# Performance work log

Hardware: AMD Instinct MI355X
Metric: run time of the kernel (lower is better)

The kernel has to match this reference:

```python
import jax, jax.numpy as jnp
import numpy as np

B, N, C = 2, 65536, 256
H, D, S = 8, 64, 64  # heads, dim_head, slice_num
INNER = H * D


def setup_inputs() -> dict:
    key = jax.random.key(0)
    ks = jax.random.split(key, 8)
    scale_in = 1.0 / np.sqrt(C)
    scale_d = 1.0 / np.sqrt(D)
    return {
        "x": jax.random.normal(ks[0], (B, N, C), dtype=jnp.float32),
        "W_x": jax.random.uniform(ks[1], (C, INNER), jnp.float32, -scale_in, scale_in),
        "b_x": jax.random.uniform(ks[2], (INNER,), jnp.float32, -scale_in, scale_in),
        "W_fx": jax.random.uniform(ks[3], (C, INNER), jnp.float32, -scale_in, scale_in),
        "b_fx": jax.random.uniform(ks[4], (INNER,), jnp.float32, -scale_in, scale_in),
        "W_slice": jax.random.uniform(ks[5], (D, S), jnp.float32, -scale_d, scale_d),
        "b_slice": jax.random.uniform(ks[6], (S,), jnp.float32, -scale_d, scale_d),
        "temperature": jnp.full((1, H, 1, 1), 0.5, dtype=jnp.float32),
    }


def _split_heads(t):
    # (B, N, H*D) -> (B, H, N, D)
    return t.reshape(B, N, H, D).transpose(0, 2, 1, 3)


def reference(x, W_x, b_x, W_fx, b_fx, W_slice, b_slice, temperature):
    projected_x = _split_heads(x @ W_x + b_x)          # (B,H,N,D)
    fx = _split_heads(x @ W_fx + b_fx)                 # (B,H,N,D)
    slice_proj = projected_x @ W_slice + b_slice       # (B,H,N,S)
    temp = jnp.clip(temperature, 0.5, 5.0)
    slice_weights = jax.nn.softmax(slice_proj / temp, axis=-1)  # (B,H,N,S)
    slice_norm = slice_weights.sum(axis=2)             # (B,H,S)
    normed = slice_weights / (slice_norm[:, :, None, :] + 0.01)
    # weighted token aggregation: (B,H,S,D)
    slice_tokens = jnp.einsum("bhns,bhnd->bhsd", normed, fx)
    return slice_tokens
```

## Files before the change

### kernel.cpp

```cpp
#include <hip/hip_runtime.h>

typedef _Float16 f16;
typedef __attribute__((ext_vector_type(8))) _Float16 f16x8;
typedef __attribute__((ext_vector_type(4))) _Float16 f16x4;
typedef __attribute__((ext_vector_type(4))) float    f32x4;

#define MFMA(a,b,c) __builtin_amdgcn_mfma_f32_16x16x32_f16(a,b,c,0,0,0)

constexpr int Bc = 2, Nc = 65536, Cc = 256, Hc = 8;
constexpr int CHUNK = 512;
constexpr int LDX = 72;
constexpr int LDT = 136;

constexpr size_t X16_OFF = 1048576;
constexpr size_t WS_BIG  = X16_OFF + (size_t)131072 * 256 * 2;

__device__ __forceinline__ f32x4 splat4(float v) { f32x4 r; r.x=v; r.y=v; r.z=v; r.w=v; return r; }
__device__ __forceinline__ f16x8 pack8(float4 a, float4 b) {
  f16x8 r = { (f16)a.x,(f16)a.y,(f16)a.z,(f16)a.w,(f16)b.x,(f16)b.y,(f16)b.z,(f16)b.w };
  return r;
}

__device__ __forceinline__ void gl_lds16(const f16* g, f16* l) {
  __builtin_amdgcn_global_load_lds((const __attribute__((address_space(1))) void*)g,
                                   (__attribute__((address_space(3))) void*)l, 16, 0, 0);
}
__device__ __forceinline__ void bar_lgkm() {
  asm volatile("s_waitcnt lgkmcnt(0)" ::: "memory");
  __builtin_amdgcn_s_barrier();
  __builtin_amdgcn_sched_barrier(0);
}
template<int N> __device__ __forceinline__ void bar_vm() {
  __builtin_amdgcn_sched_barrier(0);
  asm volatile("s_waitcnt vmcnt(%0)" :: "i"(N) : "memory");
  __builtin_amdgcn_s_barrier();
  __builtin_amdgcn_sched_barrier(0);
}

__global__ void prep_b(const float* __restrict__ x, const float* __restrict__ Wx,
                       const float* __restrict__ Wfx, const float* __restrict__ Wsl,
                       const float* __restrict__ bx, const float* __restrict__ bsl,
                       f16* __restrict__ WC, float* __restrict__ bsp,
                       float* __restrict__ Tz, f16* __restrict__ x16, int cvt_blocks) {
  __shared__ float tile[64][72];
  int b = blockIdx.x;
  const int t = threadIdx.x;
  if (b < cvt_blocks) {
    const long i = ((long)b * 256 + t) * 8;
    float4 a = *(const float4*)&x[i];
    float4 c = *(const float4*)&x[i + 4];
    *(f16x8*)&x16[i] = pack8(a, c);
    return;
  }
  b -= cvt_blocks;
  if (b < 32) {
    const int k0 = (b & 3) * 64, c0 = (b >> 2) * 64;
    const int r = t >> 4, c4 = (t & 15) * 4;
    #pragma unroll
    for (int i = 0; i < 4; ++i) {
      float4 v = *(const float4*)&Wfx[(size_t)(k0 + r + i*16)*512 + c0 + c4];
      tile[r + i*16][c4] = v.x; tile[r + i*16][c4+1] = v.y;
      tile[r + i*16][c4+2] = v.z; tile[r + i*16][c4+3] = v.w;
    }
    __syncthreads();
    const int cl = t >> 2, kq = t & 3;
    const int col = c0 + cl, h = col >> 6, n = col & 63;
    f16 tmp[16];
    #pragma unroll
    for (int jj = 0; jj < 16; ++jj) tmp[jj] = (f16)tile[kq*16 + jj][cl];
    f16* dst = WC + (size_t)(h*128 + n)*256 + k0 + kq*16;
    *(f16x8*)dst       = *(f16x8*)&tmp[0];
    *(f16x8*)(dst + 8) = *(f16x8*)&tmp[8];
  } else if (b < 96) {
    const int bb = b - 32;
    const int h = bb >> 3, k0 = (bb & 7) * 32;
    const int k = t & 31, sq = t >> 5;
    float accs[8];
    #pragma unroll
    for (int jj = 0; jj < 8; ++jj) accs[jj] = 0.f;
    for (int d = 0; d < 64; ++d) {
      float a = Wx[(size_t)(k0 + k)*512 + h*64 + d];
      #pragma unroll
      for (int jj = 0; jj < 8; ++jj) accs[jj] += a * Wsl[d*64 + sq*8 + jj];
    }
    #pragma unroll
    for (int jj = 0; jj < 8; ++jj)
      WC[(size_t)(h*128 + 64 + sq*8 + jj)*256 + k0 + k] = (f16)accs[jj];
  } else if (b == 96) {
    for (int u = t; u < 512; u += 256) {
      int h = u >> 6, s = u & 63;
      float a = bsl[s];
      for (int d = 0; d < 64; ++d) a += bx[h*64 + d] * Wsl[d*64 + s];
      bsp[h*64 + s] = a;
    }
  } else {
    float4 z; z.x = z.y = z.z = z.w = 0.f;
    ((float4*)Tz)[(b - 97) * 256 + t] = z;
  }
}

__global__ __launch_bounds__(256, 1)
void fused_dma(const f16* __restrict__ x16, const float* __restrict__ bfx,
               const float* __restrict__ bsp, const float* __restrict__ temp,
               const f16* __restrict__ WC,   float* __restrict__ Tg,
               float* __restrict__ normg) {
  __shared__ alignas(1024) f16 smem[32768];
  f16* X0 = smem;          f16* W0 = smem +  8192;
  f16* X1 = smem + 16384;  f16* W1 = smem + 24576;
  f16* sm_fxT = X1;
  f16* sm_wT  = W1;

  const int j    = blockIdx.x;
  const int xcd  = j & 7, slot = j >> 3;
  const int chunk = xcd * 32 + (slot >> 3);
  const int h     = slot & 7;

  const int tid = threadIdx.x;
  const int wv = tid >> 6, lane = tid & 63, quad = lane >> 4, ln = lane & 15;
  const int wm = wv >> 1, wn = wv & 1;
  const long tokBase = (long)chunk * CHUNK;
  const int b  = (int)(tokBase >> 16);
  const int bh = b * Hc + h;

  const float tc = fminf(fmaxf(temp[h], 0.5f), 5.0f);
  const float k2 = 1.44269504f / tc;

  float bv[4];
  {
    const float* bb = (wn == 0) ? (bfx + h*64) : (bsp + h*64);
    #pragma unroll
    for (int nt = 0; nt < 4; ++nt) bv[nt] = bb[nt*16 + ln];
  }

  f32x4 Tacc[2][2];
  #pragma unroll
  for (int i = 0; i < 2; ++i) { Tacc[i][0] = splat4(0.f); Tacc[i][1] = splat4(0.f); }
  float nacc[4] = {0.f, 0.f, 0.f, 0.f};
  const int ci = wv >> 1, cj = wv & 1;

  const f16* WCh = WC + (size_t)h * 128 * 256;

  const int l8 = lane >> 3;
  const int sl = (lane & 7) ^ l8;
  const f16* xg = x16 + (tokBase + wv*32 + l8) * 256 + sl*8;
  const f16* wg = WCh + (wv*32 + l8) * 256 + sl*8;

  auto stage = [&](int tt) {
    f16* bx_ = (tt & 1) ? X1 : X0;
    f16* bw_ = (tt & 1) ? W1 : W0;
    const f16* gx = xg + (long)(tt >> 2) * (128*256) + (tt & 3) * 64;
    const f16* gw = wg + (tt & 3) * 64;
    f16* lx = bx_ + wv * 2048;
    f16* lw = bw_ + wv * 2048;
    #pragma unroll
    for (int i = 0; i < 4; ++i) {
      gl_lds16(gx + i*2048, lx + i*512);
      gl_lds16(gw + i*2048, lw + i*512);
    }
  };

  const int swl = (ln & 7) * 8;
  const int swt = ln * 8;

  stage(0);

  for (int m0 = 0; m0 < 4; ++m0) {
    f32x4 acc[4][4];
    #pragma unroll
    for (int mt = 0; mt < 4; ++mt)
      #pragma unroll
      for (int nt = 0; nt < 4; ++nt) acc[mt][nt] = splat4(bv[nt]);

    #pragma unroll
    for (int kb = 0; kb < 4; ++kb) {
      const int t = m0*4 + kb;
      if (m0 == 3 && kb == 3) { bar_vm<0>(); }
      else                    { stage(t + 1); bar_vm<8>(); }
      const f16* sx = (t & 1) ? X1 : X0;
      const f16* sw = (t & 1) ? W1 : W0;
      #pragma unroll
      for (int ks = 0; ks < 2; ++ks) {
        f16x8 af[4], bf[4];
        #pragma unroll
        for (int mt = 0; mt < 4; ++mt)
          af[mt] = *(const f16x8*)&sx[(wm*64 + mt*16 + ln)*64 + ((ks*32 + quad*8) ^ swl)];
        #pragma unroll
        for (int nt = 0; nt < 4; ++nt)
          bf[nt] = *(const f16x8*)&sw[(wn*64 + nt*16 + ln)*64 + ((ks*32 + quad*8) ^ swl)];
        #pragma unroll
        for (int mt = 0; mt < 4; ++mt)
          #pragma unroll
          for (int nt = 0; nt < 4; ++nt)
            acc[mt][nt] = MFMA(af[mt], bf[nt], acc[mt][nt]);
      }
      bar_lgkm();
    }

    if (wn == 0) {
      #pragma unroll
      for (int mt = 0; mt < 4; ++mt)
        #pragma unroll
        for (int nt = 0; nt < 4; ++nt) {
          f16x4 v = { (f16)acc[mt][nt][0], (f16)acc[mt][nt][1],
                      (f16)acc[mt][nt][2], (f16)acc[mt][nt][3] };
          *(f16x4*)&sm_fxT[(nt*16 + ln)*128 + ((wm*64 + mt*16 + quad*4) ^ swt)] = v;
        }
    } else {
      #pragma unroll
      for (int mt = 0; mt < 4; ++mt) {
        float e[4][4], wout[4][4];
        #pragma unroll
        for (int nt = 0; nt < 4; ++nt)
          #pragma unroll
          for (int rg = 0; rg < 4; ++rg)
            e[nt][rg] = exp2f(acc[mt][nt][rg] * k2);
        #pragma unroll
        for (int rg = 0; rg < 4; ++rg) {
          float rs = e[0][rg] + e[1][rg] + e[2][rg] + e[3][rg];
          #pragma unroll
          for (int dd = 1; dd < 16; dd <<= 1) rs += __shfl_xor(rs, dd, 64);
          float inv = 1.0f / rs;
          #pragma unroll
          for (int nt = 0; nt < 4; ++nt) {
            wout[nt][rg] = e[nt][rg] * inv;
            nacc[nt] += wout[nt][rg];
          }
        }
        #pragma unroll
        for (int nt = 0; nt < 4; ++nt) {
          f16x4 v = { (f16)wout[nt][0], (f16)wout[nt][1],
                      (f16)wout[nt][2], (f16)wout[nt][3] };
          *(f16x4*)&sm_wT[(nt*16 + ln)*128 + ((wm*64 + mt*16 + quad*4) ^ swt)] = v;
        }
      }
    }
    bar_lgkm();

    #pragma unroll
    for (int ks = 0; ks < 4; ++ks) {
      f16x8 a0 = *(const f16x8*)&sm_wT [(ci*32 +      ln)*128 + ((ks*32 + quad*8) ^ swt)];
      f16x8 a1 = *(const f16x8*)&sm_wT [(ci*32 + 16 + ln)*128 + ((ks*32 + quad*8) ^ swt)];
      f16x8 b0 = *(const f16x8*)&sm_fxT[(cj*32 +      ln)*128 + ((ks*32 + quad*8) ^ swt)];
      f16x8 b1 = *(const f16x8*)&sm_fxT[(cj*32 + 16 + ln)*128 + ((ks*32 + quad*8) ^ swt)];
      Tacc[0][0] = MFMA(a0, b0, Tacc[0][0]);
      Tacc[0][1] = MFMA(a0, b1, Tacc[0][1]);
      Tacc[1][0] = MFMA(a1, b0, Tacc[1][0]);
      Tacc[1][1] = MFMA(a1, b1, Tacc[1][1]);
    }
    bar_lgkm();
  }

  float* Tb = Tg + bh * 4096;
  #pragma unroll
  for (int mt2 = 0; mt2 < 2; ++mt2)
    #pragma unroll
    for (int nt2 = 0; nt2 < 2; ++nt2)
      #pragma unroll
      for (int rg = 0; rg < 4; ++rg) {
        int s = ci*32 + mt2*16 + quad*4 + rg;
        int d = cj*32 + nt2*16 + ln;
        atomicAdd(&Tb[s*64 + d], Tacc[mt2][nt2][rg]);
      }
  if (wn == 1) {
    #pragma unroll
    for (int nt = 0; nt < 4; ++nt) {
      float v = nacc[nt];
      v += __shfl_xor(v, 16, 64);
      v += __shfl_xor(v, 32, 64);
      if (lane < 16) atomicAdd(&normg[bh*64 + nt*16 + ln], v);
    }
  }
}

__device__ __forceinline__ void wave_bar() {
  asm volatile("s_waitcnt lgkmcnt(0)" ::: "memory");
  __builtin_amdgcn_s_barrier();
  __builtin_amdgcn_sched_barrier(0);
}
__global__ __launch_bounds__(256, 2)
void fused_reg(const float* __restrict__ x,   const float* __restrict__ bfx,
               const float* __restrict__ bsp, const float* __restrict__ temp,
               const f16* __restrict__ WC,    float* __restrict__ Tg,
               float* __restrict__ normg) {
  __shared__ alignas(16) char smem[4 * 128 * LDX * 2];
  f16* X0 = (f16*)smem;
  f16* W0 = X0 + 128 * LDX;
  f16* X1 = W0 + 128 * LDX;
  f16* W1 = X1 + 128 * LDX;
  f16* sm_fxT = X1;
  f16* sm_wT  = W1;

  const int j    = blockIdx.x;
  const int xcd  = j & 7, slot = j >> 3;
  const int chunk = xcd * 32 + (slot >> 3);
  const int h     = slot & 7;

  const int tid = threadIdx.x;
  const int wv = tid >> 6, lane = tid & 63, quad = lane >> 4, ln = lane & 15;
  const int wm = wv >> 1, wn = wv & 1;
  const long tokBase = (long)chunk * CHUNK;
  const int b  = (int)(tokBase >> 16);
  const int bh = b * Hc + h;

  const float tc = fminf(fmaxf(temp[h], 0.5f), 5.0f);
  const float k2 = 1.44269504f / tc;

  float bv[4];
  {
    const float* bb = (wn == 0) ? (bfx + h*64) : (bsp + h*64);
    #pragma unroll
    for (int nt = 0; nt < 4; ++nt) bv[nt] = bb[nt*16 + ln];
  }

  f32x4 Tacc[2][2];
  #pragma unroll
  for (int i = 0; i < 2; ++i) { Tacc[i][0] = splat4(0.f); Tacc[i][1] = splat4(0.f); }
  float nacc[4] = {0.f, 0.f, 0.f, 0.f};
  const int ci = wv >> 1, cj = wv & 1;

  const f16* WCh = WC + (size_t)h * 128 * 256;
  const int r0 = tid >> 2, seg = tid & 3;
  const int wrow = tid >> 1, whalf = tid & 1;

  float4 xr[8]; f16x8 wr[4];
  auto loadx = [&](int m0, int kb) {
    const float* p = x + (tokBase + (long)m0*128 + r0)*Cc + kb*64 + seg*16;
    xr[0] = *(const float4*)p;        xr[1] = *(const float4*)(p + 4);
    xr[2] = *(const float4*)(p + 8);  xr[3] = *(const float4*)(p + 12);
    p += 64 * Cc;
    xr[4] = *(const float4*)p;        xr[5] = *(const float4*)(p + 4);
    xr[6] = *(const float4*)(p + 8);  xr[7] = *(const float4*)(p + 12);
  };
  auto loadw = [&](int kb) {
    const f16* p = WCh + wrow*256 + kb*64 + whalf*32;
    wr[0] = *(const f16x8*)p;         wr[1] = *(const f16x8*)(p + 8);
    wr[2] = *(const f16x8*)(p + 16);  wr[3] = *(const f16x8*)(p + 24);
  };

  loadx(0, 0); loadw(0);

  for (int m0 = 0; m0 < 4; ++m0) {
    f32x4 acc[4][4];
    #pragma unroll
    for (int mt = 0; mt < 4; ++mt)
      #pragma unroll
      for (int nt = 0; nt < 4; ++nt) acc[mt][nt] = splat4(bv[nt]);

    for (int kb = 0; kb < 4; ++kb) {
      const int t = m0*4 + kb;
      f16* sx = (t & 1) ? X1 : X0;
      f16* sw = (t & 1) ? W1 : W0;
      *(f16x8*)&sx[r0*LDX + seg*16]          = pack8(xr[0], xr[1]);
      *(f16x8*)&sx[r0*LDX + seg*16 + 8]      = pack8(xr[2], xr[3]);
      *(f16x8*)&sx[(r0+64)*LDX + seg*16]     = pack8(xr[4], xr[5]);
      *(f16x8*)&sx[(r0+64)*LDX + seg*16 + 8] = pack8(xr[6], xr[7]);
      *(f16x8*)&sw[wrow*LDX + whalf*32]      = wr[0];
      *(f16x8*)&sw[wrow*LDX + whalf*32 +  8] = wr[1];
      *(f16x8*)&sw[wrow*LDX + whalf*32 + 16] = wr[2];
      *(f16x8*)&sw[wrow*LDX + whalf*32 + 24] = wr[3];
      { int nt_ = t + 1;
        if (nt_ < 16) { loadx(nt_ >> 2, nt_ & 3); loadw(nt_ & 3); } }
      wave_bar();
      #pragma unroll
      for (int ks = 0; ks < 2; ++ks) {
        f16x8 af[4], bf[4];
        #pragma unroll
        for (int mt = 0; mt < 4; ++mt)
          af[mt] = *(const f16x8*)&sx[(wm*64 + mt*16 + ln)*LDX + ks*32 + quad*8];
        #pragma unroll
        for (int nt = 0; nt < 4; ++nt)
          bf[nt] = *(const f16x8*)&sw[(wn*64 + nt*16 + ln)*LDX + ks*32 + quad*8];
        #pragma unroll
        for (int mt = 0; mt < 4; ++mt)
          #pragma unroll
          for (int nt = 0; nt < 4; ++nt)
            acc[mt][nt] = MFMA(af[mt], bf[nt], acc[mt][nt]);
      }
    }
    wave_bar();

    if (wn == 0) {
      #pragma unroll
      for (int mt = 0; mt < 4; ++mt)
        #pragma unroll
        for (int nt = 0; nt < 4; ++nt) {
          f16x4 v = { (f16)acc[mt][nt][0], (f16)acc[mt][nt][1],
                      (f16)acc[mt][nt][2], (f16)acc[mt][nt][3] };
          *(f16x4*)&sm_fxT[(nt*16 + ln)*LDT + wm*64 + mt*16 + quad*4] = v;
        }
    } else {
      #pragma unroll
      for (int mt = 0; mt < 4; ++mt) {
        float e[4][4], wout[4][4];
        #pragma unroll
        for (int nt = 0; nt < 4; ++nt)
          #pragma unroll
          for (int rg = 0; rg < 4; ++rg)
            e[nt][rg] = exp2f(acc[mt][nt][rg] * k2);
        #pragma unroll
        for (int rg = 0; rg < 4; ++rg) {
          float rs = e[0][rg] + e[1][rg] + e[2][rg] + e[3][rg];
          #pragma unroll
          for (int dd = 1; dd < 16; dd <<= 1) rs += __shfl_xor(rs, dd, 64);
          float inv = 1.0f / rs;
          #pragma unroll
          for (int nt = 0; nt < 4; ++nt) {
            wout[nt][rg] = e[nt][rg] * inv;
            nacc[nt] += wout[nt][rg];
          }
        }
        #pragma unroll
        for (int nt = 0; nt < 4; ++nt) {
          f16x4 v = { (f16)wout[nt][0], (f16)wout[nt][1],
                      (f16)wout[nt][2], (f16)wout[nt][3] };
          *(f16x4*)&sm_wT[(nt*16 + ln)*LDT + wm*64 + mt*16 + quad*4] = v;
        }
      }
    }
    wave_bar();

    #pragma unroll
    for (int ks = 0; ks < 4; ++ks) {
      f16x8 a0 = *(const f16x8*)&sm_wT [(ci*32 +      ln)*LDT + ks*32 + quad*8];
      f16x8 a1 = *(const f16x8*)&sm_wT [(ci*32 + 16 + ln)*LDT + ks*32 + quad*8];
      f16x8 b0 = *(const f16x8*)&sm_fxT[(cj*32 +      ln)*LDT + ks*32 + quad*8];
      f16x8 b1 = *(const f16x8*)&sm_fxT[(cj*32 + 16 + ln)*LDT + ks*32 + quad*8];
      Tacc[0][0] = MFMA(a0, b0, Tacc[0][0]);
      Tacc[0][1] = MFMA(a0, b1, Tacc[0][1]);
      Tacc[1][0] = MFMA(a1, b0, Tacc[1][0]);
      Tacc[1][1] = MFMA(a1, b1, Tacc[1][1]);
    }
  }

  float* Tb = Tg + bh * 4096;
  #pragma unroll
  for (int mt2 = 0; mt2 < 2; ++mt2)
    #pragma unroll
    for (int nt2 = 0; nt2 < 2; ++nt2)
      #pragma unroll
      for (int rg = 0; rg < 4; ++rg) {
        int s = ci*32 + mt2*16 + quad*4 + rg;
        int d = cj*32 + nt2*16 + ln;
        atomicAdd(&Tb[s*64 + d], Tacc[mt2][nt2][rg]);
      }
  if (wn == 1) {
    #pragma unroll
    for (int nt = 0; nt < 4; ++nt) {
      float v = nacc[nt];
      v += __shfl_xor(v, 16, 64);
      v += __shfl_xor(v, 32, 64);
      if (lane < 16) atomicAdd(&normg[bh*64 + nt*16 + ln], v);
    }
  }
}

__global__ void finalize(const float* __restrict__ Tg, const float* __restrict__ normg,
                         float* __restrict__ out) {
  int i = blockIdx.x * 256 + threadIdx.x;
  out[i] = Tg[i] / (normg[i >> 6] + 0.01f);
}

extern "C" void kernel_launch(void* const* d_in, const int* in_sizes, int n_in,
                              void* d_out, int out_size, void* d_ws, size_t ws_size,
                              hipStream_t stream) {
  const float* x    = (const float*)d_in[0];
  const float* Wx   = (const float*)d_in[1];
  const float* bx   = (const float*)d_in[2];
  const float* Wfx  = (const float*)d_in[3];
  const float* bfx  = (const float*)d_in[4];
  const float* Wsl  = (const float*)d_in[5];
  const float* bsl  = (const float*)d_in[6];
  const float* temp = (const float*)d_in[7];
  float* out = (float*)d_out;

  float* Tg    = (float*)d_ws;
  float* normg = Tg + 16 * 4096;
  f16*   WC    = (f16*)((char*)d_ws + 266240);
  float* bsp   = (float*)((char*)d_ws + 790528);
  f16*   x16   = (f16*)((char*)d_ws + X16_OFF);

  if (ws_size >= WS_BIG) {
    prep_b   <<<16384 + 162, 256, 0, stream>>>(x, Wx, Wfx, Wsl, bx, bsl, WC, bsp, Tg, x16, 16384);
    fused_dma<<<2048, 256, 0, stream>>>(x16, bfx, bsp, temp, WC, Tg, normg);
  } else {
    prep_b   <<<162, 256, 0, stream>>>(x, Wx, Wfx, Wsl, bx, bsl, WC, bsp, Tg, x16, 0);
    fused_reg<<<2048, 256, 0, stream>>>(x, bfx, bsp, temp, WC, Tg, normg);
  }
  finalize <<<256, 256, 0, stream>>>(Tg, normg, out);
}
```

Before: 411.6 us.

## Load each x chunk once per block and loop over all heads in-block

Drops the separate fp32-to-fp16 pass over x into workspace and the per-(chunk,head) grid. Each of 256 blocks now converts a 128-token tile of x straight into a large LDS buffer once, then iterates over all 8 heads, streaming double-buffered weight tiles. This removes reading x eight times and the extra conversion kernel. The cost is only 256 blocks with about 136KB of LDS each, so occupancy is low, and atomics to Tg are now issued per head per sub-tile, which increases atomic traffic. An unused fused_all kernel is left in the file.

New measurement: 441.3 us. +7.2%, slower.

```diff
diff --git a/kernel.cpp b/kernel.cpp
--- a/kernel.cpp
+++ b/kernel.cpp
@@ -9,50 +9,36 @@
 
 constexpr int Bc = 2, Nc = 65536, Cc = 256, Hc = 8;
 constexpr int CHUNK = 512;
-constexpr int LDX = 72;
-constexpr int LDT = 136;
-
-constexpr size_t X16_OFF = 1048576;
-constexpr size_t WS_BIG  = X16_OFF + (size_t)131072 * 256 * 2;
+constexpr int LDXX = 264;
+constexpr int LDT  = 136;
+
 
 __device__ __forceinline__ f32x4 splat4(float v) { f32x4 r; r.x=v; r.y=v; r.z=v; r.w=v; return r; }
 __device__ __forceinline__ f16x8 pack8(float4 a, float4 b) {
   f16x8 r = { (f16)a.x,(f16)a.y,(f16)a.z,(f16)a.w,(f16)b.x,(f16)b.y,(f16)b.z,(f16)b.w };
   return r;
 }
-
 __device__ __forceinline__ void gl_lds16(const f16* g, f16* l) {
   __builtin_amdgcn_global_load_lds((const __attribute__((address_space(1))) void*)g,
                                    (__attribute__((address_space(3))) void*)l, 16, 0, 0);
+}
+__device__ __forceinline__ void bar_all() {
+  asm volatile("s_waitcnt vmcnt(0) lgkmcnt(0)" ::: "memory");
+  __builtin_amdgcn_s_barrier();
+  __builtin_amdgcn_sched_barrier(0);
 }
 __device__ __forceinline__ void bar_lgkm() {
   asm volatile("s_waitcnt lgkmcnt(0)" ::: "memory");
   __builtin_amdgcn_s_barrier();
   __builtin_amdgcn_sched_barrier(0);
 }
-template<int N> __device__ __forceinline__ void bar_vm() {
-  __builtin_amdgcn_sched_barrier(0);
-  asm volatile("s_waitcnt vmcnt(%0)" :: "i"(N) : "memory");
-  __builtin_amdgcn_s_barrier();
-  __builtin_amdgcn_sched_barrier(0);
-}
-
-__global__ void prep_b(const float* __restrict__ x, const float* __restrict__ Wx,
-                       const float* __restrict__ Wfx, const float* __restrict__ Wsl,
-                       const float* __restrict__ bx, const float* __restrict__ bsl,
-                       f16* __restrict__ WC, float* __restrict__ bsp,
-                       float* __restrict__ Tz, f16* __restrict__ x16, int cvt_blocks) {
+
+__global__ void prep_a(const float* __restrict__ Wx, const float* __restrict__ Wfx,
+                       const float* __restrict__ Wsl, const float* __restrict__ bx,
+                       const float* __restrict__ bsl, f16* __restrict__ WC,
+                       float* __restrict__ bsp, float* __restrict__ Tz) {
   __shared__ float tile[64][72];
-  int b = blockIdx.x;
-  const int t = threadIdx.x;
-  if (b < cvt_blocks) {
-    const long i = ((long)b * 256 + t) * 8;
-    float4 a = *(const float4*)&x[i];
-    float4 c = *(const float4*)&x[i + 4];
-    *(f16x8*)&x16[i] = pack8(a, c);
-    return;
-  }
-  b -= cvt_blocks;
+  const int b = blockIdx.x, t = threadIdx.x;
   if (b < 32) {
     const int k0 = (b & 3) * 64, c0 = (b >> 2) * 64;
     const int r = t >> 4, c4 = (t & 15) * 4;
@@ -67,7 +53,7 @@
     const int col = c0 + cl, h = col >> 6, n = col & 63;
     f16 tmp[16];
     #pragma unroll
-    for (int jj = 0; jj < 16; ++jj) tmp[jj] = (f16)tile[kq*16 + jj][cl];
+    for (int j = 0; j < 16; ++j) tmp[j] = (f16)tile[kq*16 + j][cl];
     f16* dst = WC + (size_t)(h*128 + n)*256 + k0 + kq*16;
     *(f16x8*)dst       = *(f16x8*)&tmp[0];
     *(f16x8*)(dst + 8) = *(f16x8*)&tmp[8];
@@ -77,15 +63,15 @@
     const int k = t & 31, sq = t >> 5;
     float accs[8];
     #pragma unroll
-    for (int jj = 0; jj < 8; ++jj) accs[jj] = 0.f;
+    for (int j = 0; j < 8; ++j) accs[j] = 0.f;
     for (int d = 0; d < 64; ++d) {
       float a = Wx[(size_t)(k0 + k)*512 + h*64 + d];
       #pragma unroll
-      for (int jj = 0; jj < 8; ++jj) accs[jj] += a * Wsl[d*64 + sq*8 + jj];
-    }
-    #pragma unroll
-    for (int jj = 0; jj < 8; ++jj)
-      WC[(size_t)(h*128 + 64 + sq*8 + jj)*256 + k0 + k] = (f16)accs[jj];
+      for (int j = 0; j < 8; ++j) accs[j] += a * Wsl[d*64 + sq*8 + j];
+    }
+    #pragma unroll
+    for (int j = 0; j < 8; ++j)
+      WC[(size_t)(h*128 + 64 + sq*8 + j)*256 + k0 + k] = (f16)accs[j];
   } else if (b == 96) {
     for (int u = t; u < 512; u += 256) {
       int h = u >> 6, s = u & 63;
@@ -100,356 +86,343 @@
 }
 
 __global__ __launch_bounds__(256, 1)
-void fused_dma(const f16* __restrict__ x16, const float* __restrict__ bfx,
+void fused_all(const float* __restrict__ x,   const float* __restrict__ bfx,
                const float* __restrict__ bsp, const float* __restrict__ temp,
-               const f16* __restrict__ WC,   float* __restrict__ Tg,
+               const f16* __restrict__ WC,    float* __restrict__ Tg,
                float* __restrict__ normg) {
-  __shared__ alignas(1024) f16 smem[32768];
-  f16* X0 = smem;          f16* W0 = smem +  8192;
-  f16* X1 = smem + 16384;  f16* W1 = smem + 24576;
-  f16* sm_fxT = X1;
-  f16* sm_wT  = W1;
-
-  const int j    = blockIdx.x;
-  const int xcd  = j & 7, slot = j >> 3;
-  const int chunk = xcd * 32 + (slot >> 3);
-  const int h     = slot & 7;
+  __shared__ alignas(1024) char smem[136192];
+  f16* X      = (f16*)smem;
+  f16* W0     = (f16*)(smem + 68608);
+  f16* W1     = (f16*)(smem + 84992);
+  f16* sm_fxT = (f16*)(smem + 101376);
+  f16* sm_wT  = (f16*)(smem + 118784);
+
+  const int chunk = blockIdx.x;
+  const long tokBase = (long)chunk * CHUNK;
+  const int b = (int)(tokBase >> 16);
 
   const int tid = threadIdx.x;
   const int wv = tid >> 6, lane = tid & 63, quad = lane >> 4, ln = lane & 15;
   const int wm = wv >> 1, wn = wv & 1;
+  const int ci = wv >> 1, cj = wv & 1;
+  const int r0 = tid >> 2, seg = tid & 3;
+  const int l8 = lane >> 3, sl = (lane & 7) ^ l8;
+  const int swl = (ln & 7) * 8;
+
+  auto stageW = [&](int h, int kb, int p) {
+    f16* dst = (p ? W1 : W0) + wv * 2048;
+    const f16* src = WC + ((size_t)(h*128 + wv*32 + l8))*256 + kb*64 + sl*8;
+    #pragma unroll
+    for (int i = 0; i < 4; ++i)
+      gl_lds16(src + i*(8*256), dst + i*512);
+  };
+
+  auto stageX = [&](int m0) {
+    const float* p = x + (tokBase + (long)m0*128 + r0)*Cc + seg*16;
+    #pragma unroll
+    for (int kb = 0; kb < 4; ++kb) {
+      const float* q  = p + kb*64;
+      const float* q2 = q + 64*Cc;
+      float4 a0 = *(const float4*)q,      a1 = *(const float4*)(q+4);
+      float4 a2 = *(const float4*)(q+8),  a3 = *(const float4*)(q+12);
+      float4 b0 = *(const float4*)q2,     b1 = *(const float4*)(q2+4);
+      float4 b2 = *(const float4*)(q2+8), b3 = *(const float4*)(q2+12);
+      *(f16x8*)&X[r0*LDXX + kb*64 + seg*16]          = pack8(a0, a1);
+      *(f16x8*)&X[r0*LDXX + kb*64 + seg*16 + 8]      = pack8(a2, a3);
+      *(f16x8*)&X[(r0+64)*LDXX + kb*64 + seg*16]     = pack8(b0, b1);
+      *(f16x8*)&X[(r0+64)*LDXX + kb*64 + seg*16 + 8] = pack8(b2, b3);
+    }
+  };
+
+  #pragma unroll 1
+  for (int m0 = 0; m0 < 4; ++m0) {
+    stageX(m0);
+    stageW(0, 0, 0);
+
+    #pragma unroll 1
+    for (int h = 0; h < 8; ++h) {
+      const float tc = fminf(fmaxf(temp[h], 0.5f), 5.0f);
+      const float k2 = 1.44269504f / tc;
+      float bv[4];
+      {
+        const float* bb = (wn == 0) ? (bfx + h*64) : (bsp + h*64);
+        #pragma unroll
+        for (int nt = 0; nt < 4; ++nt) bv[nt] = bb[nt*16 + ln];
+      }
+
+      f32x4 acc[4][4];
+      #pragma unroll
+      for (int mt = 0; mt < 4; ++mt)
+        #pragma unroll
+        for (int nt = 0; nt < 4; ++nt) acc[mt][nt] = splat4(bv[nt]);
+
+      #pragma unroll
+      for (int kb = 0; kb < 4; ++kb) {
+        bar_all();
+        if (kb < 3)       stageW(h, kb + 1, (kb + 1) & 1);
+        else if (h < 7)   stageW(h + 1, 0, 0);
+        const f16* Wb = (kb & 1) ? W1 : W0;
+        #pragma unroll
+        for (int ks = 0; ks < 2; ++ks) {
+          f16x8 af[4], bf[4];
+          #pragma unroll
+          for (int mt = 0; mt < 4; ++mt)
+            af[mt] = *(const f16x8*)&X[(wm*64 + mt*16 + ln)*LDXX + kb*64 + ks*32 + quad*8];
+          #pragma unroll
+          for (int nt = 0; nt < 4; ++nt)
+            bf[nt] = *(const f16x8*)&Wb[(wn*64 + nt*16 + ln)*64 + ((ks*32 + quad*8) ^ swl)];
+          #pragma unroll
+          for (int mt = 0; mt < 4; ++mt)
+            #pragma unroll
+            for (int nt = 0; nt < 4; ++nt)
+              acc[mt][nt] = MFMA(af[mt], bf[nt], acc[mt][nt]);
+        }
+      }
+
+      if (wn == 0) {
+        #pragma unroll
+        for (int mt = 0; mt < 4; ++mt)
+          #pragma unroll
+          for (int nt = 0; nt < 4; ++nt) {
+            f16x4 v = { (f16)acc[mt][nt][0], (f16)acc[mt][nt][1],
+                        (f16)acc[mt][nt][2], (f16)acc[mt][nt][3] };
+            *(f16x4*)&sm_fxT[(nt*16 + ln)*LDT + wm*64 + mt*16 + quad*4] = v;
+          }
+      } else {
+        #pragma unroll
+        for (int mt = 0; mt < 4; ++mt) {
+          float e[4][4], wout[4][4];
+          #pragma unroll
+          for (int nt = 0; nt < 4; ++nt)
+            #pragma unroll
+            for (int rg = 0; rg < 4; ++rg)
+              e[nt][rg] = exp2f(acc[mt][nt][rg] * k2);
+          #pragma unroll
+          for (int rg = 0; rg < 4; ++rg) {
+            float rs = e[0][rg] + e[1][rg] + e[2][rg] + e[3][rg];
+            #pragma unroll
+            for (int dd = 1; dd < 16; dd <<= 1) rs += __shfl_xor(rs, dd, 64);
+            float inv = 1.0f / rs;
+            #pragma unroll
+            for (int nt = 0; nt < 4; ++nt) {
+              wout[nt][rg] = e[nt][rg] * inv;
+            }
+          }
+          #pragma unroll
+          for (int nt = 0; nt < 4; ++nt) {
+            f16x4 v = { (f16)wout[nt][0], (f16)wout[nt][1],
+                        (f16)wout[nt][2], (f16)wout[nt][3] };
+            *(f16x4*)&sm_wT[(nt*16 + ln)*LDT + wm*64 + mt*16 + quad*4] = v;
+          }
+        }
+      }
+      bar_lgkm();
+
+      f32x4 Tacc[2][2];
+      #pragma unroll
+      for (int i = 0; i < 2; ++i) { Tacc[i][0] = splat4(0.f); Tacc[i][1] = splat4(0.f); }
+      float nacc[4] = {0.f, 0.f, 0.f, 0.f};
+      #pragma unroll
+      for (int ks = 0; ks < 4; ++ks) {
+        f16x8 a0 = *(const f16x8*)&sm_wT [(ci*32 +      ln)*LDT + ks*32 + quad*8];
+        f16x8 a1 = *(const f16x8*)&sm_wT [(ci*32 + 16 + ln)*LDT + ks*32 + quad*8];
+        f16x8 b0 = *(const f16x8*)&sm_fxT[(cj*32 +      ln)*LDT + ks*32 + quad*8];
+        f16x8 b1 = *(const f16x8*)&sm_fxT[(cj*32 + 16 + ln)*LDT + ks*32 + quad*8];
+        Tacc[0][0] = MFMA(a0, b0, Tacc[0][0]);
+        Tacc[0][1] = MFMA(a0, b1, Tacc[0][1]);
+        Tacc[1][0] = MFMA(a1, b0, Tacc[1][0]);
+        Tacc[1][1] = MFMA(a1, b1, Tacc[1][1]);
+      }
+      {
+        const int bh = b * Hc + h;
+        float* Tb = Tg + bh * 4096;
+        #pragma unroll
+        for (int mt2 = 0; mt2 < 2; ++mt2)
+          #pragma unroll
+          for (int nt2 = 0; nt2 < 2; ++nt2)
+            #pragma unroll
+            for (int rg = 0; rg < 4; ++rg) {
+              int s = ci*32 + mt2*16 + quad*4 + rg;
+              int d = cj*32 + nt2*16 + ln;
+              atomicAdd(&Tb[s*64 + d], Tacc[mt2][nt2][rg]);
+            }
+        (void)nacc;
+      }
+    }
+  }
+}
+
+
+__global__ __launch_bounds__(256, 1)
+void fused_all2(const float* __restrict__ x,   const float* __restrict__ bfx,
+                const float* __restrict__ bsp, const float* __restrict__ temp,
+                const f16* __restrict__ WC,    float* __restrict__ Tg,
+                float* __restrict__ normg) {
+  __shared__ alignas(1024) char smem[136192];
+  f16* X      = (f16*)smem;
+  f16* W0     = (f16*)(smem + 68608);
+  f16* W1     = (f16*)(smem + 84992);
+  f16* sm_fxT = (f16*)(smem + 101376);
+  f16* sm_wT  = (f16*)(smem + 118784);
+
+  const int chunk = blockIdx.x;
   const long tokBase = (long)chunk * CHUNK;
-  const int b  = (int)(tokBase >> 16);
-  const int bh = b * Hc + h;
-
-  const float tc = fminf(fmaxf(temp[h], 0.5f), 5.0f);
-  const float k2 = 1.44269504f / tc;
-
-  float bv[4];
-  {
-    const float* bb = (wn == 0) ? (bfx + h*64) : (bsp + h*64);
-    #pragma unroll
-    for (int nt = 0; nt < 4; ++nt) bv[nt] = bb[nt*16 + ln];
-  }
-
-  f32x4 Tacc[2][2];
-  #pragma unroll
-  for (int i = 0; i < 2; ++i) { Tacc[i][0] = splat4(0.f); Tacc[i][1] = splat4(0.f); }
-  float nacc[4] = {0.f, 0.f, 0.f, 0.f};
-  const int ci = wv >> 1, cj = wv & 1;
-
-  const f16* WCh = WC + (size_t)h * 128 * 256;
-
-  const int l8 = lane >> 3;
-  const int sl = (lane & 7) ^ l8;
-  const f16* xg = x16 + (tokBase + wv*32 + l8) * 256 + sl*8;
-  const f16* wg = WCh + (wv*32 + l8) * 256 + sl*8;
-
-  auto stage = [&](int tt) {
-    f16* bx_ = (tt & 1) ? X1 : X0;
-    f16* bw_ = (tt & 1) ? W1 : W0;
-    const f16* gx = xg + (long)(tt >> 2) * (128*256) + (tt & 3) * 64;
-    const f16* gw = wg + (tt & 3) * 64;
-    f16* lx = bx_ + wv * 2048;
-    f16* lw = bw_ + wv * 2048;
-    #pragma unroll
-    for (int i = 0; i < 4; ++i) {
-      gl_lds16(gx + i*2048, lx + i*512);
-      gl_lds16(gw + i*2048, lw + i*512);
-    }
-  };
-
-  const int swl = (ln & 7) * 8;
-  const int swt = ln * 8;
-
-  stage(0);
-
-  for (int m0 = 0; m0 < 4; ++m0) {
-    f32x4 acc[4][4];
-    #pragma unroll
-    for (int mt = 0; mt < 4; ++mt)
-      #pragma unroll
-      for (int nt = 0; nt < 4; ++nt) acc[mt][nt] = splat4(bv[nt]);
-
-    #pragma unroll
-    for (int kb = 0; kb < 4; ++kb) {
-      const int t = m0*4 + kb;
-      if (m0 == 3 && kb == 3) { bar_vm<0>(); }
-      else                    { stage(t + 1); bar_vm<8>(); }
-      const f16* sx = (t & 1) ? X1 : X0;
-      const f16* sw = (t & 1) ? W1 : W0;
-      #pragma unroll
-      for (int ks = 0; ks < 2; ++ks) {
-        f16x8 af[4], bf[4];
-        #pragma unroll
-        for (int mt = 0; mt < 4; ++mt)
-          af[mt] = *(const f16x8*)&sx[(wm*64 + mt*16 + ln)*64 + ((ks*32 + quad*8) ^ swl)];
-        #pragma unroll
-        for (int nt = 0; nt < 4; ++nt)
-          bf[nt] = *(const f16x8*)&sw[(wn*64 + nt*16 + ln)*64 + ((ks*32 + quad*8) ^ swl)];
-        #pragma unroll
-        for (int mt = 0; mt < 4; ++mt)
-          #pragma unroll
-          for (int nt = 0; nt < 4; ++nt)
-            acc[mt][nt] = MFMA(af[mt], bf[nt], acc[mt][nt]);
-      }
-      bar_lgkm();
-    }
-
-    if (wn == 0) {
-      #pragma unroll
-      for (int mt = 0; mt < 4; ++mt)
-        #pragma unroll
-        for (int nt = 0; nt < 4; ++nt) {
-          f16x4 v = { (f16)acc[mt][nt][0], (f16)acc[mt][nt][1],
-                      (f16)acc[mt][nt][2], (f16)acc[mt][nt][3] };
-          *(f16x4*)&sm_fxT[(nt*16 + ln)*128 + ((wm*64 + mt*16 + quad*4) ^ swt)] = v;
-        }
-    } else {
-      #pragma unroll
-      for (int mt = 0; mt < 4; ++mt) {
-        float e[4][4], wout[4][4];
-        #pragma unroll
-        for (int nt = 0; nt < 4; ++nt)
-          #pragma unroll
-          for (int rg = 0; rg < 4; ++rg)
-            e[nt][rg] = exp2f(acc[mt][nt][rg] * k2);
-        #pragma unroll
-        for (int rg = 0; rg < 4; ++rg) {
-          float rs = e[0][rg] + e[1][rg] + e[2][rg] + e[3][rg];
-          #pragma unroll
-          for (int dd = 1; dd < 16; dd <<= 1) rs += __shfl_xor(rs, dd, 64);
-          float inv = 1.0f / rs;
-          #pragma unroll
-          for (int nt = 0; nt < 4; ++nt) {
-            wout[nt][rg] = e[nt][rg] * inv;
-            nacc[nt] += wout[nt][rg];
-          }
-        }
-        #pragma unroll
-        for (int nt = 0; nt < 4; ++nt) {
-          f16x4 v = { (f16)wout[nt][0], (f16)wout[nt][1],
-                      (f16)wout[nt][2], (f16)wout[nt][3] };
-          *(f16x4*)&sm_wT[(nt*16 + ln)*128 + ((wm*64 + mt*16 + quad*4) ^ swt)] = v;
-        }
-      }
-    }
-    bar_lgkm();
-
-    #pragma unroll
-    for (int ks = 0; ks < 4; ++ks) {
-      f16x8 a0 = *(const f16x8*)&sm_wT [(ci*32 +      ln)*128 + ((ks*32 + quad*8) ^ swt)];
-      f16x8 a1 = *(const f16x8*)&sm_wT [(ci*32 + 16 + ln)*128 + ((ks*32 + quad*8) ^ swt)];
-      f16x8 b0 = *(const f16x8*)&sm_fxT[(cj*32 +      ln)*128 + ((ks*32 + quad*8) ^ swt)];
-      f16x8 b1 = *(const f16x8*)&sm_fxT[(cj*32 + 16 + ln)*128 + ((ks*32 + quad*8) ^ swt)];
-      Tacc[0][0] = MFMA(a0, b0, Tacc[0][0]);
-      Tacc[0][1] = MFMA(a0, b1, Tacc[0][1]);
-      Tacc[1][0] = MFMA(a1, b0, Tacc[1][0]);
-      Tacc[1][1] = MFMA(a1, b1, Tacc[1][1]);
-    }
-    bar_lgkm();
-  }
-
-  float* Tb = Tg + bh * 4096;
-  #pragma unroll
-  for (int mt2 = 0; mt2 < 2; ++mt2)
-    #pragma unroll
-    for (int nt2 = 0; nt2 < 2; ++nt2)
-      #pragma unroll
-      for (int rg = 0; rg < 4; ++rg) {
-        int s = ci*32 + mt2*16 + quad*4 + rg;
-        int d = cj*32 + nt2*16 + ln;
-        atomicAdd(&Tb[s*64 + d], Tacc[mt2][nt2][rg]);
-      }
-  if (wn == 1) {
-    #pragma unroll
-    for (int nt = 0; nt < 4; ++nt) {
-      float v = nacc[nt];
-      v += __shfl_xor(v, 16, 64);
-      v += __shfl_xor(v, 32, 64);
-      if (lane < 16) atomicAdd(&normg[bh*64 + nt*16 + ln], v);
-    }
-  }
-}
-
-__device__ __forceinline__ void wave_bar() {
-  asm volatile("s_waitcnt lgkmcnt(0)" ::: "memory");
-  __builtin_amdgcn_s_barrier();
-  __builtin_amdgcn_sched_barrier(0);
-}
-__global__ __launch_bounds__(256, 2)
-void fused_reg(const float* __restrict__ x,   const float* __restrict__ bfx,
-               const float* __restrict__ bsp, const float* __restrict__ temp,
-               const f16* __restrict__ WC,    float* __restrict__ Tg,
-               float* __restrict__ normg) {
-  __shared__ alignas(16) char smem[4 * 128 * LDX * 2];
-  f16* X0 = (f16*)smem;
-  f16* W0 = X0 + 128 * LDX;
-  f16* X1 = W0 + 128 * LDX;
-  f16* W1 = X1 + 128 * LDX;
-  f16* sm_fxT = X1;
-  f16* sm_wT  = W1;
-
-  const int j    = blockIdx.x;
-  const int xcd  = j & 7, slot = j >> 3;
-  const int chunk = xcd * 32 + (slot >> 3);
-  const int h     = slot & 7;
+  const int b = (int)(tokBase >> 16);
 
   const int tid = threadIdx.x;
   const int wv = tid >> 6, lane = tid & 63, quad = lane >> 4, ln = lane & 15;
   const int wm = wv >> 1, wn = wv & 1;
-  const long tokBase = (long)chunk * CHUNK;
-  const int b  = (int)(tokBase >> 16);
-  const int bh = b * Hc + h;
-
-  const float tc = fminf(fmaxf(temp[h], 0.5f), 5.0f);
-  const float k2 = 1.44269504f / tc;
-
-  float bv[4];
-  {
-    const float* bb = (wn == 0) ? (bfx + h*64) : (bsp + h*64);
-    #pragma unroll
-    for (int nt = 0; nt < 4; ++nt) bv[nt] = bb[nt*16 + ln];
-  }
-
-  f32x4 Tacc[2][2];
-  #pragma unroll
-  for (int i = 0; i < 2; ++i) { Tacc[i][0] = splat4(0.f); Tacc[i][1] = splat4(0.f); }
-  float nacc[4] = {0.f, 0.f, 0.f, 0.f};
   const int ci = wv >> 1, cj = wv & 1;
-
-  const f16* WCh = WC + (size_t)h * 128 * 256;
   const int r0 = tid >> 2, seg = tid & 3;
-  const int wrow = tid >> 1, whalf = tid & 1;
-
-  float4 xr[8]; f16x8 wr[4];
-  auto loadx = [&](int m0, int kb) {
-    const float* p = x + (tokBase + (long)m0*128 + r0)*Cc + kb*64 + seg*16;
-    xr[0] = *(const float4*)p;        xr[1] = *(const float4*)(p + 4);
-    xr[2] = *(const float4*)(p + 8);  xr[3] = *(const float4*)(p + 12);
-    p += 64 * Cc;
-    xr[4] = *(const float4*)p;        xr[5] = *(const float4*)(p + 4);
-    xr[6] = *(const float4*)(p + 8);  xr[7] = *(const float4*)(p + 12);
+  const int l8 = lane >> 3, sl = (lane & 7) ^ l8;
+  const int swl = (ln & 7) * 8;
+
+  auto stageW = [&](int h, int kb, int p) {
+    f16* dst = (p ? W1 : W0) + wv * 2048;
+    const f16* src = WC + ((size_t)(h*128 + wv*32 + l8))*256 + kb*64 + sl*8;
+    #pragma unroll
+    for (int i = 0; i < 4; ++i)
+      gl_lds16(src + i*(8*256), dst + i*512);
   };
-  auto loadw = [&](int kb) {
-    const f16* p = WCh + wrow*256 + kb*64 + whalf*32;
-    wr[0] = *(const f16x8*)p;         wr[1] = *(const f16x8*)(p + 8);
-    wr[2] = *(const f16x8*)(p + 16);  wr[3] = *(const f16x8*)(p + 24);
+  auto stageX = [&](int m0) {
+    const float* p = x + (tokBase + (long)m0*128 + r0)*Cc + seg*16;
+    #pragma unroll
+    for (int kb = 0; kb < 4; ++kb) {
+      const float* q  = p + kb*64;
+      const float* q2 = q + 64*Cc;
+      float4 a0 = *(const float4*)q,      a1 = *(const float4*)(q+4);
+      float4 a2 = *(const float4*)(q+8),  a3 = *(const float4*)(q+12);
+      float4 b0 = *(const float4*)q2,     b1 = *(const float4*)(q2+4);
+      float4 b2 = *(const float4*)(q2+8), b3 = *(const float4*)(q2+12);
+      *(f16x8*)&X[r0*LDXX + kb*64 + seg*16]          = pack8(a0, a1);
+      *(f16x8*)&X[r0*LDXX + kb*64 + seg*16 + 8]      = pack8(a2, a3);
+      *(f16x8*)&X[(r0+64)*LDXX + kb*64 + seg*16]     = pack8(b0, b1);
+      *(f16x8*)&X[(r0+64)*LDXX + kb*64 + seg*16 + 8] = pack8(b2, b3);
+    }
   };
 
-  loadx(0, 0); loadw(0);
-
+  #pragma unroll 1
   for (int m0 = 0; m0 < 4; ++m0) {
-    f32x4 acc[4][4];
-    #pragma unroll
-    for (int mt = 0; mt < 4; ++mt)
-      #pragma unroll
-      for (int nt = 0; nt < 4; ++nt) acc[mt][nt] = splat4(bv[nt]);
-
-    for (int kb = 0; kb < 4; ++kb) {
-      const int t = m0*4 + kb;
-      f16* sx = (t & 1) ? X1 : X0;
-      f16* sw = (t & 1) ? W1 : W0;
-      *(f16x8*)&sx[r0*LDX + seg*16]          = pack8(xr[0], xr[1]);
-      *(f16x8*)&sx[r0*LDX + seg*16 + 8]      = pack8(xr[2], xr[3]);
-      *(f16x8*)&sx[(r0+64)*LDX + seg*16]     = pack8(xr[4], xr[5]);
-      *(f16x8*)&sx[(r0+64)*LDX + seg*16 + 8] = pack8(xr[6], xr[7]);
-      *(f16x8*)&sw[wrow*LDX + whalf*32]      = wr[0];
-      *(f16x8*)&sw[wrow*LDX + whalf*32 +  8] = wr[1];
-      *(f16x8*)&sw[wrow*LDX + whalf*32 + 16] = wr[2];
-      *(f16x8*)&sw[wrow*LDX + whalf*32 + 24] = wr[3];
-      { int nt_ = t + 1;
-        if (nt_ < 16) { loadx(nt_ >> 2, nt_ & 3); loadw(nt_ & 3); } }
-      wave_bar();
-      #pragma unroll
-      for (int ks = 0; ks < 2; ++ks) {
-        f16x8 af[4], bf[4];
+    stageX(m0);
+    stageW(0, 0, 0);
+
+    #pragma unroll 1
+    for (int h = 0; h < 8; ++h) {
+      const float tc = fminf(fmaxf(temp[h], 0.5f), 5.0f);
+      const float k2 = 1.44269504f / tc;
+      float bv[4];
+      {
+        const float* bb = (wn == 0) ? (bfx + h*64) : (bsp + h*64);
+        #pragma unroll
+        for (int nt = 0; nt < 4; ++nt) bv[nt] = bb[nt*16 + ln];
+      }
+
+      f32x4 acc[4][4];
+      #pragma unroll
+      for (int mt = 0; mt < 4; ++mt)
+        #pragma unroll
+        for (int nt = 0; nt < 4; ++nt) acc[mt][nt] = splat4(bv[nt]);
+
+      #pragma unroll
+      for (int kb = 0; kb < 4; ++kb) {
+        bar_all();
+        if (kb < 3)      stageW(h, kb + 1, (kb + 1) & 1);
+        else if (h < 7)  stageW(h + 1, 0, 0);
+        const f16* Wb = (kb & 1) ? W1 : W0;
+        #pragma unroll
+        for (int ks = 0; ks < 2; ++ks) {
+          f16x8 af[4], bf[4];
+          #pragma unroll
+          for (int mt = 0; mt < 4; ++mt)
+            af[mt] = *(const f16x8*)&X[(wm*64 + mt*16 + ln)*LDXX + kb*64 + ks*32 + quad*8];
+          #pragma unroll
+          for (int nt = 0; nt < 4; ++nt)
+            bf[nt] = *(const f16x8*)&Wb[(wn*64 + nt*16 + ln)*64 + ((ks*32 + quad*8) ^ swl)];
+          #pragma unroll
+          for (int mt = 0; mt < 4; ++mt)
+            #pragma unroll
+            for (int nt = 0; nt < 4; ++nt)
+              acc[mt][nt] = MFMA(af[mt], bf[nt], acc[mt][nt]);
+        }
+      }
+
+      float nacc[4] = {0.f, 0.f, 0.f, 0.f};
+      if (wn == 0) {
         #pragma unroll
         for (int mt = 0; mt < 4; ++mt)
-          af[mt] = *(const f16x8*)&sx[(wm*64 + mt*16 + ln)*LDX + ks*32 + quad*8];
-        #pragma unroll
-        for (int nt = 0; nt < 4; ++nt)
-          bf[nt] = *(const f16x8*)&sw[(wn*64 + nt*16 + ln)*LDX + ks*32 + quad*8];
-        #pragma unroll
-        for (int mt = 0; mt < 4; ++mt)
+          #pragma unroll
+          for (int nt = 0; nt < 4; ++nt) {
+            f16x4 v = { (f16)acc[mt][nt][0], (f16)acc[mt][nt][1],
+                        (f16)acc[mt][nt][2], (f16)acc[mt][nt][3] };
+            *(f16x4*)&sm_fxT[(nt*16 + ln)*LDT + wm*64 + mt*16 + quad*4] = v;
+          }
+      } else {
+        #pragma unroll
+        for (int mt = 0; mt < 4; ++mt) {
+          float e[4][4], wout[4][4];
           #pragma unroll
           for (int nt = 0; nt < 4; ++nt)
-            acc[mt][nt] = MFMA(af[mt], bf[nt], acc[mt][nt]);
-      }
-    }
-    wave_bar();
-
-    if (wn == 0) {
-      #pragma unroll
-      for (int mt = 0; mt < 4; ++mt)
+            #pragma unroll
+            for (int rg = 0; rg < 4; ++rg)
+              e[nt][rg] = exp2f(acc[mt][nt][rg] * k2);
+          #pragma unroll
+          for (int rg = 0; rg < 4; ++rg) {
+            float rs = e[0][rg] + e[1][rg] + e[2][rg] + e[3][rg];
+            #pragma unroll
+            for (int dd = 1; dd < 16; dd <<= 1) rs += __shfl_xor(rs, dd, 64);
+            float inv = 1.0f / rs;
+            #pragma unroll
+            for (int nt = 0; nt < 4; ++nt) {
+              wout[nt][rg] = e[nt][rg] * inv;
+              nacc[nt] += wout[nt][rg];
+            }
+          }
+          #pragma unroll
+          for (int nt = 0; nt < 4; ++nt) {
+            f16x4 v = { (f16)wout[nt][0], (f16)wout[nt][1],
+                        (f16)wout[nt][2], (f16)wout[nt][3] };
+            *(f16x4*)&sm_wT[(nt*16 + ln)*LDT + wm*64 + mt*16 + quad*4] = v;
+          }
+        }
+      }
+      bar_lgkm();
+
+      f32x4 Tacc[2][2];
+      #pragma unroll
+      for (int i = 0; i < 2; ++i) { Tacc[i][0] = splat4(0.f); Tacc[i][1] = splat4(0.f); }
+      #pragma unroll
+      for (int ks = 0; ks < 4; ++ks) {
+        f16x8 a0 = *(const f16x8*)&sm_wT [(ci*32 +      ln)*LDT + ks*32 + quad*8];
+        f16x8 a1 = *(const f16x8*)&sm_wT [(ci*32 + 16 + ln)*LDT + ks*32 + quad*8];
+        f16x8 b0 = *(const f16x8*)&sm_fxT[(cj*32 +      ln)*LDT + ks*32 + quad*8];
+        f16x8 b1 = *(const f16x8*)&sm_fxT[(cj*32 + 16 + ln)*LDT + ks*32 + quad*8];
+        Tacc[0][0] = MFMA(a0, b0, Tacc[0][0]);
+        Tacc[0][1] = MFMA(a0, b1, Tacc[0][1]);
+        Tacc[1][0] = MFMA(a1, b0, Tacc[1][0]);
+        Tacc[1][1] = MFMA(a1, b1, Tacc[1][1]);
+      }
+
+      const int bh = b * Hc + h;
+      float* Tb = Tg + bh * 4096;
+      #pragma unroll
+      for (int mt2 = 0; mt2 < 2; ++mt2)
+        #pragma unroll
+        for (int nt2 = 0; nt2 < 2; ++nt2)
+          #pragma unroll
+          for (int rg = 0; rg < 4; ++rg) {
+            int s = ci*32 + mt2*16 + quad*4 + rg;
+            int d = cj*32 + nt2*16 + ln;
+            atomicAdd(&Tb[s*64 + d], Tacc[mt2][nt2][rg]);
+          }
+      if (wn == 1) {
         #pragma unroll
         for (int nt = 0; nt < 4; ++nt) {
-          f16x4 v = { (f16)acc[mt][nt][0], (f16)acc[mt][nt][1],
-                      (f16)acc[mt][nt][2], (f16)acc[mt][nt][3] };
-          *(f16x4*)&sm_fxT[(nt*16 + ln)*LDT + wm*64 + mt*16 + quad*4] = v;
+          float v = nacc[nt];
+          v += __shfl_xor(v, 16, 64);
+          v += __shfl_xor(v, 32, 64);
+          if (lane < 16) atomicAdd(&normg[bh*64 + nt*16 + ln], v);
         }
-    } else {
-      #pragma unroll
-      for (int mt = 0; mt < 4; ++mt) {
-        float e[4][4], wout[4][4];
-        #pragma unroll
-        for (int nt = 0; nt < 4; ++nt)
-          #pragma unroll
-          for (int rg = 0; rg < 4; ++rg)
-            e[nt][rg] = exp2f(acc[mt][nt][rg] * k2);
-        #pragma unroll
-        for (int rg = 0; rg < 4; ++rg) {
-          float rs = e[0][rg] + e[1][rg] + e[2][rg] + e[3][rg];
-          #pragma unroll
-          for (int dd = 1; dd < 16; dd <<= 1) rs += __shfl_xor(rs, dd, 64);
-          float inv = 1.0f / rs;
-          #pragma unroll
-          for (int nt = 0; nt < 4; ++nt) {
-            wout[nt][rg] = e[nt][rg] * inv;
-            nacc[nt] += wout[nt][rg];
-          }
-        }
-        #pragma unroll
-        for (int nt = 0; nt < 4; ++nt) {
-          f16x4 v = { (f16)wout[nt][0], (f16)wout[nt][1],
-                      (f16)wout[nt][2], (f16)wout[nt][3] };
-          *(f16x4*)&sm_wT[(nt*16 + ln)*LDT + wm*64 + mt*16 + quad*4] = v;
-        }
-      }
-    }
-    wave_bar();
-
-    #pragma unroll
-    for (int ks = 0; ks < 4; ++ks) {
-      f16x8 a0 = *(const f16x8*)&sm_wT [(ci*32 +      ln)*LDT + ks*32 + quad*8];
-      f16x8 a1 = *(const f16x8*)&sm_wT [(ci*32 + 16 + ln)*LDT + ks*32 + quad*8];
-      f16x8 b0 = *(const f16x8*)&sm_fxT[(cj*32 +      ln)*LDT + ks*32 + quad*8];
-      f16x8 b1 = *(const f16x8*)&sm_fxT[(cj*32 + 16 + ln)*LDT + ks*32 + quad*8];
-      Tacc[0][0] = MFMA(a0, b0, Tacc[0][0]);
-      Tacc[0][1] = MFMA(a0, b1, Tacc[0][1]);
-      Tacc[1][0] = MFMA(a1, b0, Tacc[1][0]);
-      Tacc[1][1] = MFMA(a1, b1, Tacc[1][1]);
-    }
-  }
-
-  float* Tb = Tg + bh * 4096;
-  #pragma unroll
-  for (int mt2 = 0; mt2 < 2; ++mt2)
-    #pragma unroll
-    for (int nt2 = 0; nt2 < 2; ++nt2)
-      #pragma unroll
-      for (int rg = 0; rg < 4; ++rg) {
-        int s = ci*32 + mt2*16 + quad*4 + rg;
-        int d = cj*32 + nt2*16 + ln;
-        atomicAdd(&Tb[s*64 + d], Tacc[mt2][nt2][rg]);
-      }
-  if (wn == 1) {
-    #pragma unroll
-    for (int nt = 0; nt < 4; ++nt) {
-      float v = nacc[nt];
-      v += __shfl_xor(v, 16, 64);
-      v += __shfl_xor(v, 32, 64);
-      if (lane < 16) atomicAdd(&normg[bh*64 + nt*16 + ln], v);
+      }
     }
   }
 }
@@ -477,14 +450,8 @@
   float* normg = Tg + 16 * 4096;
   f16*   WC    = (f16*)((char*)d_ws + 266240);
   float* bsp   = (float*)((char*)d_ws + 790528);
-  f16*   x16   = (f16*)((char*)d_ws + X16_OFF);
-
-  if (ws_size >= WS_BIG) {
-    prep_b   <<<16384 + 162, 256, 0, stream>>>(x, Wx, Wfx, Wsl, bx, bsl, WC, bsp, Tg, x16, 16384);
-    fused_dma<<<2048, 256, 0, stream>>>(x16, bfx, bsp, temp, WC, Tg, normg);
-  } else {
-    prep_b   <<<162, 256, 0, stream>>>(x, Wx, Wfx, Wsl, bx, bsl, WC, bsp, Tg, x16, 0);
-    fused_reg<<<2048, 256, 0, stream>>>(x, bfx, bsp, temp, WC, Tg, normg);
-  }
-  finalize <<<256, 256, 0, stream>>>(Tg, normg, out);
-}
+
+  prep_a    <<<162, 256, 0, stream>>>(Wx, Wfx, Wsl, bx, bsl, WC, bsp, Tg);
+  fused_all2<<<256, 256, 0, stream>>>(x, bfx, bsp, temp, WC, Tg, normg);
+  finalize  <<<256, 256, 0, stream>>>(Tg, normg, out);
+}
```
